# Optimization experiments

Measured on AMD Instinct MI355X. Metric: run time of the kernel, lower is better.

The kernel has to match this reference:

```python
import jax, jax.numpy as jnp
import numpy as np

B, N, IN_F, OUT_F = 32, 1024, 256, 256


def setup_inputs() -> dict:
    key = jax.random.key(0)
    k_adj, k_feat, k_w, k_b = jax.random.split(key, 4)
    adjacency = jax.random.uniform(k_adj, (B, N, N), dtype=jnp.float32)  # [B,N,N]
    features = jax.random.normal(k_feat, (B, N, IN_F), dtype=jnp.float32)  # [B,N,in]
    # 'thomas' init ~ uniform(-1/sqrt(fan_in), 1/sqrt(fan_in)) style; scale is
    # irrelevant to correctness-checking, use scaled normal.
    weight = jax.random.normal(k_w, (IN_F, OUT_F), dtype=jnp.float32) / np.sqrt(IN_F)
    bias = jax.random.normal(k_b, (OUT_F,), dtype=jnp.float32) / np.sqrt(IN_F)
    return {"adjacency": adjacency, "features": features, "weight": weight, "bias": bias}


def reference(adjacency, features, weight, bias) -> jnp.ndarray:
    # support = features @ weight : [B,N,out]
    support = jnp.einsum("bni,io->bno", features, weight)
    # output = bmm(adjacency, support) : [B,N,out]
    output = jnp.einsum("bnm,bmo->bno", adjacency, support)
    return output + bias
```

## Files before the change

kernel.cpp:

```cpp
#include <hip/hip_runtime.h>
#include <hip/hip_bf16.h>


typedef __attribute__((__ext_vector_type__(4))) float  f32x4;
typedef __attribute__((__ext_vector_type__(8))) __bf16 bf16x8;
typedef __attribute__((__ext_vector_type__(4))) __bf16 bf16x4;

#define BM 64
#define BN 256
#define BK 32

__device__ __forceinline__ void gld16(const void* g, void* l) {
  __builtin_amdgcn_global_load_lds(
      (const __attribute__((address_space(1))) unsigned int*)g,
      (__attribute__((address_space(3))) unsigned int*)l, 16, 0, 0);
}

__global__ __launch_bounds__(256) void k_wt(const float* __restrict__ w,
                                            __bf16* __restrict__ Wt) {
  __shared__ __bf16 T[64][65];
  const int bi = blockIdx.x >> 2;
  const int bj = blockIdx.x & 3;
  const int t  = threadIdx.x;
  const int r  = t >> 2;
  const int q  = t & 3;
  const float* src = w + (size_t)(bi * 64 + r) * 256 + bj * 64 + q * 16;
#pragma unroll
  for (int u = 0; u < 4; ++u) {
    f32x4 v = *(const f32x4*)(src + u * 4);
    T[r][q * 16 + u * 4 + 0] = (__bf16)v[0];
    T[r][q * 16 + u * 4 + 1] = (__bf16)v[1];
    T[r][q * 16 + u * 4 + 2] = (__bf16)v[2];
    T[r][q * 16 + u * 4 + 3] = (__bf16)v[3];
  }
  __syncthreads();
  bf16x8 h0, h1;
#pragma unroll
  for (int u = 0; u < 8; ++u) {
    h0[u] = T[q * 16 + u][r];
    h1[u] = T[q * 16 + 8 + u][r];
  }
  __bf16* d0 = Wt + ((size_t)(bi * 8 + q * 2) * 256 + (bj * 64 + r)) * 8;
  *(bf16x8*)d0          = h0;
  *(bf16x8*)(d0 + 2048) = h1;
}

template <int KTOT, int LDA, bool EPI_ST>
__global__ __launch_bounds__(512, 4) void k_gemm(
    const float* __restrict__ Aall, const __bf16* __restrict__ Bg_all,
    const float* __restrict__ bias, float* __restrict__ Out,
    __bf16* __restrict__ St) {
  __shared__ float  Af[2][BM * BK];
  __shared__ __bf16 Bf[2][4 * BN * 8];

  const int tid  = threadIdx.x;
  const int lane = tid & 63;
  const int wid  = tid >> 6;
  const int wr   = wid >> 2;
  const int wc   = wid & 3;
  const int l16  = lane & 15;
  const int g    = lane >> 4;

  int b, mtile;
  const float*  Ablk;
  const __bf16* Bblk;
  if constexpr (EPI_ST) {
    const int lg = blockIdx.x;
    b     = lg >> 4;
    mtile = lg & 15;
    Ablk  = Aall + (size_t)lg * BM * LDA;
    Bblk  = Bg_all;
  } else {
    const int h  = blockIdx.x;
    const int lg = (h & 7) * 64 + (h >> 3);
    b     = lg >> 4;
    mtile = lg & 15;
    Ablk  = Aall + (size_t)b * 1024 * 1024 + (size_t)mtile * BM * LDA;
    Bblk  = Bg_all + (size_t)b * 262144;
  }

  const int    ar   = tid >> 3;
  const float* asrc = Ablk + (size_t)ar * LDA + (((tid & 7) ^ (ar & 7)) << 2);
  const __bf16* bs0 = Bblk + ((size_t)wid * 128 + lane) * 8;

  auto stage = [&](int buf, int k0) {
    gld16(asrc + k0, &Af[buf][wid * 256]);
    const __bf16* bt = bs0 + (size_t)(k0 >> 3) * 2048;
    gld16(bt,       &Bf[buf][wid * 1024]);
    gld16(bt + 512, &Bf[buf][wid * 1024 + 512]);
  };

  f32x4 acc[2][4];
#pragma unroll
  for (int m = 0; m < 2; ++m)
#pragma unroll
    for (int n = 0; n < 4; ++n) acc[m][n] = (f32x4){0.f, 0.f, 0.f, 0.f};

  const int h7 = l16 & 7;
  auto compute = [&](int buf) {
    bf16x8 af[2], bv[4];
#pragma unroll
    for (int m = 0; m < 2; ++m) {
      const float* base = &Af[buf][(wr * 32 + m * 16 + l16) * BK];
      f32x4 v0 = *(const f32x4*)(base + (((2 * g)     ^ h7) << 2));
      f32x4 v1 = *(const f32x4*)(base + (((2 * g + 1) ^ h7) << 2));
      af[m] = (bf16x8){(__bf16)v0[0], (__bf16)v0[1], (__bf16)v0[2], (__bf16)v0[3],
                       (__bf16)v1[0], (__bf16)v1[1], (__bf16)v1[2], (__bf16)v1[3]};
    }
#pragma unroll
    for (int n = 0; n < 4; ++n)
      bv[n] = *(const bf16x8*)&Bf[buf][(g * 256 + wc * 64 + n * 16 + l16) * 8];
#pragma unroll
    for (int m = 0; m < 2; ++m)
#pragma unroll
      for (int n = 0; n < 4; ++n)
        acc[m][n] = __builtin_amdgcn_mfma_f32_16x16x32_bf16(af[m], bv[n], acc[m][n], 0, 0, 0);
  };

  constexpr int NT = KTOT / BK;
  stage(0, 0);
  __syncthreads();
  for (int t = 0; t < NT - 2; t += 2) {
    stage(1, (t + 1) * BK);
    compute(0);
    __syncthreads();
    stage(0, (t + 2) * BK);
    compute(1);
    __syncthreads();
  }
  stage(1, (NT - 1) * BK);
  compute(0);
  __syncthreads();
  compute(1);

  const int rg = (lane >> 4) * 4;
  if constexpr (EPI_ST) {
    __bf16* Stb = St + (size_t)b * 262144;
#pragma unroll
    for (int n = 0; n < 4; ++n) {
      const int col = wc * 64 + n * 16 + l16;
#pragma unroll
      for (int m = 0; m < 2; ++m) {
        const int gm = mtile * 64 + wr * 32 + m * 16 + rg;
        __bf16* dst = Stb + ((size_t)(gm >> 3) * 256 + col) * 8 + (gm & 7);
        bf16x4 hh = {(__bf16)acc[m][n][0], (__bf16)acc[m][n][1],
                     (__bf16)acc[m][n][2], (__bf16)acc[m][n][3]};
        *(bf16x4*)dst = hh;
      }
    }
  } else {
    float* ob = Out + ((size_t)b * 1024 + (size_t)mtile * BM) * 256;
#pragma unroll
    for (int n = 0; n < 4; ++n) {
      const int col = wc * 64 + n * 16 + l16;
      const float bvs = bias[col];
#pragma unroll
      for (int m = 0; m < 2; ++m) {
        const int row = wr * 32 + m * 16 + rg;
#pragma unroll
        for (int r2 = 0; r2 < 4; ++r2)
          ob[(size_t)(row + r2) * 256 + col] = acc[m][n][r2] + bvs;
      }
    }
  }
}

extern "C" void kernel_launch(void* const* d_in, const int* in_sizes, int n_in,
                              void* d_out, int out_size, void* d_ws, size_t ws_size,
                              hipStream_t stream) {
  const float* adj  = (const float*)d_in[0];
  const float* feat = (const float*)d_in[1];
  const float* w    = (const float*)d_in[2];
  const float* bias = (const float*)d_in[3];
  float* out = (float*)d_out;

  __bf16* Wt = (__bf16*)d_ws;
  __bf16* St = (__bf16*)((char*)d_ws + 131072);

  k_wt<<<16, 256, 0, stream>>>(w, Wt);
  k_gemm<256, 256, true><<<512, 512, 0, stream>>>(feat, Wt, nullptr, nullptr, St);
  k_gemm<1024, 1024, false><<<512, 512, 0, stream>>>(adj, St, bias, out, nullptr);
}
```

Measured before the change: 54.37 us.

## Replace LDS-staged GEMM with direct global-to-register double-buffered loads

New measurement: 73.33 us. 1.35x slower.

```diff
diff --git a/kernel.cpp b/kernel.cpp
--- a/kernel.cpp
+++ b/kernel.cpp
@@ -6,15 +6,7 @@
 typedef __attribute__((__ext_vector_type__(8))) __bf16 bf16x8;
 typedef __attribute__((__ext_vector_type__(4))) __bf16 bf16x4;
 
-#define BM 64
-#define BN 256
 #define BK 32
-
-__device__ __forceinline__ void gld16(const void* g, void* l) {
-  __builtin_amdgcn_global_load_lds(
-      (const __attribute__((address_space(1))) unsigned int*)g,
-      (__attribute__((address_space(3))) unsigned int*)l, 16, 0, 0);
-}
 
 __global__ __launch_bounds__(256) void k_wt(const float* __restrict__ w,
                                             __bf16* __restrict__ Wt) {
@@ -46,117 +38,113 @@
 }
 
 template <int KTOT, int LDA, bool EPI_ST>
-__global__ __launch_bounds__(512, 4) void k_gemm(
+__global__ __launch_bounds__(256, 2) void k_gemm(
     const float* __restrict__ Aall, const __bf16* __restrict__ Bg_all,
     const float* __restrict__ bias, float* __restrict__ Out,
     __bf16* __restrict__ St) {
-  __shared__ float  Af[2][BM * BK];
-  __shared__ __bf16 Bf[2][4 * BN * 8];
-
   const int tid  = threadIdx.x;
   const int lane = tid & 63;
-  const int wid  = tid >> 6;
-  const int wr   = wid >> 2;
-  const int wc   = wid & 3;
+  const int w    = tid >> 6;
   const int l16  = lane & 15;
   const int g    = lane >> 4;
 
-  int b, mtile;
+  int b, mblk;
   const float*  Ablk;
   const __bf16* Bblk;
   if constexpr (EPI_ST) {
-    const int lg = blockIdx.x;
-    b     = lg >> 4;
-    mtile = lg & 15;
-    Ablk  = Aall + (size_t)lg * BM * LDA;
-    Bblk  = Bg_all;
+    const int bx = blockIdx.x;
+    b    = bx >> 4;
+    mblk = bx & 15;
+    Ablk = Aall + (size_t)bx * 64 * LDA;
+    Bblk = Bg_all;
   } else {
     const int h  = blockIdx.x;
     const int lg = (h & 7) * 64 + (h >> 3);
-    b     = lg >> 4;
-    mtile = lg & 15;
-    Ablk  = Aall + (size_t)b * 1024 * 1024 + (size_t)mtile * BM * LDA;
-    Bblk  = Bg_all + (size_t)b * 262144;
+    b    = lg >> 4;
+    mblk = lg & 15;
+    Ablk = Aall + (size_t)b * 1024 * 1024 + (size_t)mblk * 64 * LDA;
+    Bblk = Bg_all + (size_t)b * 262144;
   }
 
-  const int    ar   = tid >> 3;
-  const float* asrc = Ablk + (size_t)ar * LDA + (((tid & 7) ^ (ar & 7)) << 2);
-  const __bf16* bs0 = Bblk + ((size_t)wid * 128 + lane) * 8;
+  const int wm = (w >> 1) * 32;
+  const int nb = (w & 1) * 128;
 
-  auto stage = [&](int buf, int k0) {
-    gld16(asrc + k0, &Af[buf][wid * 256]);
-    const __bf16* bt = bs0 + (size_t)(k0 >> 3) * 2048;
-    gld16(bt,       &Bf[buf][wid * 1024]);
-    gld16(bt + 512, &Bf[buf][wid * 1024 + 512]);
+  const float* arow0 = Ablk + (size_t)(wm + l16) * LDA + g * 8;
+  const float* arow1 = arow0 + (size_t)16 * LDA;
+  const __bf16* bl = Bblk + (size_t)g * 2048 + (size_t)(nb + l16) * 8;
+
+  f32x4  a0[4], a1[4];
+  bf16x8 b0[8], b1[8];
+
+  auto issueA = [&](f32x4* a, int k0) {
+    a[0] = *(const f32x4*)(arow0 + k0);
+    a[1] = *(const f32x4*)(arow0 + k0 + 4);
+    a[2] = *(const f32x4*)(arow1 + k0);
+    a[3] = *(const f32x4*)(arow1 + k0 + 4);
+  };
+  auto issueB = [&](bf16x8* bb, int k0) {
+    const __bf16* p = bl + (size_t)(k0 >> 3) * 2048;
+#pragma unroll
+    for (int n = 0; n < 8; ++n) bb[n] = *(const bf16x8*)(p + n * 128);
   };
 
-  f32x4 acc[2][4];
+  f32x4 acc[2][8];
 #pragma unroll
   for (int m = 0; m < 2; ++m)
 #pragma unroll
-    for (int n = 0; n < 4; ++n) acc[m][n] = (f32x4){0.f, 0.f, 0.f, 0.f};
+    for (int n = 0; n < 8; ++n) acc[m][n] = (f32x4){0.f, 0.f, 0.f, 0.f};
 
-  const int h7 = l16 & 7;
-  auto compute = [&](int buf) {
-    bf16x8 af[2], bv[4];
+  auto step = [&](const f32x4* a, const bf16x8* bb) {
+    bf16x8 af0 = {(__bf16)a[0][0], (__bf16)a[0][1], (__bf16)a[0][2], (__bf16)a[0][3],
+                  (__bf16)a[1][0], (__bf16)a[1][1], (__bf16)a[1][2], (__bf16)a[1][3]};
+    bf16x8 af1 = {(__bf16)a[2][0], (__bf16)a[2][1], (__bf16)a[2][2], (__bf16)a[2][3],
+                  (__bf16)a[3][0], (__bf16)a[3][1], (__bf16)a[3][2], (__bf16)a[3][3]};
 #pragma unroll
-    for (int m = 0; m < 2; ++m) {
-      const float* base = &Af[buf][(wr * 32 + m * 16 + l16) * BK];
-      f32x4 v0 = *(const f32x4*)(base + (((2 * g)     ^ h7) << 2));
-      f32x4 v1 = *(const f32x4*)(base + (((2 * g + 1) ^ h7) << 2));
-      af[m] = (bf16x8){(__bf16)v0[0], (__bf16)v0[1], (__bf16)v0[2], (__bf16)v0[3],
-                       (__bf16)v1[0], (__bf16)v1[1], (__bf16)v1[2], (__bf16)v1[3]};
+    for (int n = 0; n < 8; ++n) {
+      acc[0][n] = __builtin_amdgcn_mfma_f32_16x16x32_bf16(af0, bb[n], acc[0][n], 0, 0, 0);
+      acc[1][n] = __builtin_amdgcn_mfma_f32_16x16x32_bf16(af1, bb[n], acc[1][n], 0, 0, 0);
     }
-#pragma unroll
-    for (int n = 0; n < 4; ++n)
-      bv[n] = *(const bf16x8*)&Bf[buf][(g * 256 + wc * 64 + n * 16 + l16) * 8];
-#pragma unroll
-    for (int m = 0; m < 2; ++m)
-#pragma unroll
-      for (int n = 0; n < 4; ++n)
-        acc[m][n] = __builtin_amdgcn_mfma_f32_16x16x32_bf16(af[m], bv[n], acc[m][n], 0, 0, 0);
   };
 
   constexpr int NT = KTOT / BK;
-  stage(0, 0);
-  __syncthreads();
+  issueA(a0, 0);   issueB(b0, 0);
+  issueA(a1, BK);  issueB(b1, BK);
   for (int t = 0; t < NT - 2; t += 2) {
-    stage(1, (t + 1) * BK);
-    compute(0);
-    __syncthreads();
-    stage(0, (t + 2) * BK);
-    compute(1);
-    __syncthreads();
+    step(a0, b0);
+    issueA(a0, (t + 2) * BK);
+    issueB(b0, (t + 2) * BK);
+    step(a1, b1);
+    issueA(a1, (t + 3) * BK);
+    issueB(b1, (t + 3) * BK);
   }
-  stage(1, (NT - 1) * BK);
-  compute(0);
-  __syncthreads();
-  compute(1);
+  step(a0, b0);
+  step(a1, b1);
 
-  const int rg = (lane >> 4) * 4;
+  const int rg = g * 4;
   if constexpr (EPI_ST) {
     __bf16* Stb = St + (size_t)b * 262144;
+    const int gm0 = mblk * 64 + wm;
 #pragma unroll
-    for (int n = 0; n < 4; ++n) {
-      const int col = wc * 64 + n * 16 + l16;
+    for (int n = 0; n < 8; ++n) {
+      const int col = nb + n * 16 + l16;
 #pragma unroll
       for (int m = 0; m < 2; ++m) {
-        const int gm = mtile * 64 + wr * 32 + m * 16 + rg;
-        __bf16* dst = Stb + ((size_t)(gm >> 3) * 256 + col) * 8 + (gm & 7);
+        const int gm = gm0 + m * 16 + rg;
+        __bf16* dst = Stb + (size_t)(gm >> 3) * 2048 + (size_t)col * 8 + (gm & 7);
         bf16x4 hh = {(__bf16)acc[m][n][0], (__bf16)acc[m][n][1],
                      (__bf16)acc[m][n][2], (__bf16)acc[m][n][3]};
         *(bf16x4*)dst = hh;
       }
     }
   } else {
-    float* ob = Out + ((size_t)b * 1024 + (size_t)mtile * BM) * 256;
+    float* ob = Out + ((size_t)b * 1024 + (size_t)mblk * 64 + wm) * 256;
 #pragma unroll
-    for (int n = 0; n < 4; ++n) {
-      const int col = wc * 64 + n * 16 + l16;
+    for (int n = 0; n < 8; ++n) {
+      const int col = nb + n * 16 + l16;
       const float bvs = bias[col];
 #pragma unroll
       for (int m = 0; m < 2; ++m) {
-        const int row = wr * 32 + m * 16 + rg;
+        const int row = m * 16 + rg;
 #pragma unroll
         for (int r2 = 0; r2 < 4; ++r2)
           ob[(size_t)(row + r2) * 256 + col] = acc[m][n][r2] + bvs;
@@ -178,6 +166,6 @@
   __bf16* St = (__bf16*)((char*)d_ws + 131072);
 
   k_wt<<<16, 256, 0, stream>>>(w, Wt);
-  k_gemm<256, 256, true><<<512, 512, 0, stream>>>(feat, Wt, nullptr, nullptr, St);
-  k_gemm<1024, 1024, false><<<512, 512, 0, stream>>>(adj, St, bias, out, nullptr);
+  k_gemm<256, 256, true><<<512, 256, 0, stream>>>(feat, Wt, nullptr, nullptr, St);
+  k_gemm<1024, 1024, false><<<512, 256, 0, stream>>>(adj, St, bias, out, nullptr);
 }
```

## Enlarge GEMM tiles to 128x256 with BK=64 and halve grid size

Applied to the files above, without the earlier changes.

Measured after the change: 54.09 us. Within noise of the previous version (-0.5%).

```diff
diff --git a/kernel.cpp b/kernel.cpp
--- a/kernel.cpp
+++ b/kernel.cpp
@@ -6,9 +6,7 @@
 typedef __attribute__((__ext_vector_type__(8))) __bf16 bf16x8;
 typedef __attribute__((__ext_vector_type__(4))) __bf16 bf16x4;
 
-#define BM 64
-#define BN 256
-#define BK 32
+#define BK 64
 
 __device__ __forceinline__ void gld16(const void* g, void* l) {
   __builtin_amdgcn_global_load_lds(
@@ -46,12 +44,12 @@
 }
 
 template <int KTOT, int LDA, bool EPI_ST>
-__global__ __launch_bounds__(512, 4) void k_gemm(
+__global__ __launch_bounds__(512, 2) void k_gemm(
     const float* __restrict__ Aall, const __bf16* __restrict__ Bg_all,
     const float* __restrict__ bias, float* __restrict__ Out,
     __bf16* __restrict__ St) {
-  __shared__ float  Af[2][BM * BK];
-  __shared__ __bf16 Bf[2][4 * BN * 8];
+  __shared__ float  Af[2][128 * 64];
+  __shared__ __bf16 Bf[2][8 * 256 * 8];
 
   const int tid  = threadIdx.x;
   const int lane = tid & 63;
@@ -61,102 +59,118 @@
   const int l16  = lane & 15;
   const int g    = lane >> 4;
 
-  int b, mtile;
+  int b, mblk;
   const float*  Ablk;
   const __bf16* Bblk;
   if constexpr (EPI_ST) {
-    const int lg = blockIdx.x;
-    b     = lg >> 4;
-    mtile = lg & 15;
-    Ablk  = Aall + (size_t)lg * BM * LDA;
-    Bblk  = Bg_all;
+    const int bx = blockIdx.x;
+    b    = bx >> 3;
+    mblk = bx & 7;
+    Ablk = Aall + (size_t)bx * 128 * LDA;
+    Bblk = Bg_all;
   } else {
     const int h  = blockIdx.x;
-    const int lg = (h & 7) * 64 + (h >> 3);
-    b     = lg >> 4;
-    mtile = lg & 15;
-    Ablk  = Aall + (size_t)b * 1024 * 1024 + (size_t)mtile * BM * LDA;
-    Bblk  = Bg_all + (size_t)b * 262144;
+    const int lg = (h & 7) * 32 + (h >> 3);
+    b    = lg >> 3;
+    mblk = lg & 7;
+    Ablk = Aall + (size_t)b * 1024 * 1024 + (size_t)mblk * 128 * LDA;
+    Bblk = Bg_all + (size_t)b * 262144;
   }
 
-  const int    ar   = tid >> 3;
-  const float* asrc = Ablk + (size_t)ar * LDA + (((tid & 7) ^ (ar & 7)) << 2);
-  const __bf16* bs0 = Bblk + ((size_t)wid * 128 + lane) * 8;
+  const float*  aS[4];
+  const __bf16* bS[4];
+#pragma unroll
+  for (int i = 0; i < 4; ++i) {
+    const int c = i * 512 + tid;
+    aS[i] = Ablk + (size_t)(c >> 4) * LDA + (((c & 15) ^ ((c >> 4) & 7)) << 2);
+    bS[i] = Bblk + (size_t)c * 8;
+  }
 
-  auto stage = [&](int buf, int k0) {
-    gld16(asrc + k0, &Af[buf][wid * 256]);
-    const __bf16* bt = bs0 + (size_t)(k0 >> 3) * 2048;
-    gld16(bt,       &Bf[buf][wid * 1024]);
-    gld16(bt + 512, &Bf[buf][wid * 1024 + 512]);
-  };
+#define STAGE(buf, k0)                                                        \
+  {                                                                           \
+    const size_t koff = (size_t)((k0) >> 3) * 2048;                           \
+    _Pragma("unroll") for (int i = 0; i < 4; ++i) {                           \
+      gld16(aS[i] + (k0), &Af[buf][(i * 512 + wid * 64) * 4]);                \
+      gld16(bS[i] + koff, &Bf[buf][(i * 512 + wid * 64) * 8]);                \
+    }                                                                         \
+  }
 
-  f32x4 acc[2][4];
+  f32x4 acc[4][4];
 #pragma unroll
-  for (int m = 0; m < 2; ++m)
+  for (int m = 0; m < 4; ++m)
 #pragma unroll
     for (int n = 0; n < 4; ++n) acc[m][n] = (f32x4){0.f, 0.f, 0.f, 0.f};
 
-  const int h7 = l16 & 7;
   auto compute = [&](int buf) {
-    bf16x8 af[2], bv[4];
 #pragma unroll
-    for (int m = 0; m < 2; ++m) {
-      const float* base = &Af[buf][(wr * 32 + m * 16 + l16) * BK];
-      f32x4 v0 = *(const f32x4*)(base + (((2 * g)     ^ h7) << 2));
-      f32x4 v1 = *(const f32x4*)(base + (((2 * g + 1) ^ h7) << 2));
-      af[m] = (bf16x8){(__bf16)v0[0], (__bf16)v0[1], (__bf16)v0[2], (__bf16)v0[3],
-                       (__bf16)v1[0], (__bf16)v1[1], (__bf16)v1[2], (__bf16)v1[3]};
+    for (int ks = 0; ks < 2; ++ks) {
+      bf16x8 af[4], bv[4];
+#pragma unroll
+      for (int m = 0; m < 4; ++m) {
+        const int row = wr * 64 + m * 16 + l16;
+        const int rx  = row & 7;
+        const int c0  = (ks * 8 + 2 * g) ^ rx;
+        const int c1  = (ks * 8 + 2 * g + 1) ^ rx;
+        f32x4 v0 = *(const f32x4*)&Af[buf][row * 64 + c0 * 4];
+        f32x4 v1 = *(const f32x4*)&Af[buf][row * 64 + c1 * 4];
+        af[m] = (bf16x8){(__bf16)v0[0], (__bf16)v0[1], (__bf16)v0[2], (__bf16)v0[3],
+                         (__bf16)v1[0], (__bf16)v1[1], (__bf16)v1[2], (__bf16)v1[3]};
+      }
+#pragma unroll
+      for (int n = 0; n < 4; ++n) {
+        const int col = wc * 64 + n * 16 + l16;
+        bv[n] = *(const bf16x8*)&Bf[buf][((ks * 4 + g) * 256 + col) * 8];
+      }
+#pragma unroll
+      for (int m = 0; m < 4; ++m)
+#pragma unroll
+        for (int n = 0; n < 4; ++n)
+          acc[m][n] = __builtin_amdgcn_mfma_f32_16x16x32_bf16(af[m], bv[n], acc[m][n], 0, 0, 0);
     }
-#pragma unroll
-    for (int n = 0; n < 4; ++n)
-      bv[n] = *(const bf16x8*)&Bf[buf][(g * 256 + wc * 64 + n * 16 + l16) * 8];
-#pragma unroll
-    for (int m = 0; m < 2; ++m)
-#pragma unroll
-      for (int n = 0; n < 4; ++n)
-        acc[m][n] = __builtin_amdgcn_mfma_f32_16x16x32_bf16(af[m], bv[n], acc[m][n], 0, 0, 0);
   };
 
   constexpr int NT = KTOT / BK;
-  stage(0, 0);
+  STAGE(0, 0);
   __syncthreads();
   for (int t = 0; t < NT - 2; t += 2) {
-    stage(1, (t + 1) * BK);
+    STAGE(1, (t + 1) * BK);
     compute(0);
     __syncthreads();
-    stage(0, (t + 2) * BK);
+    STAGE(0, (t + 2) * BK);
     compute(1);
     __syncthreads();
   }
-  stage(1, (NT - 1) * BK);
+  STAGE(1, (NT - 1) * BK);
   compute(0);
   __syncthreads();
   compute(1);
+#undef STAGE
 
-  const int rg = (lane >> 4) * 4;
+  const int rg = g * 4;
   if constexpr (EPI_ST) {
     __bf16* Stb = St + (size_t)b * 262144;
+    const int gm0 = mblk * 128 + wr * 64;
 #pragma unroll
     for (int n = 0; n < 4; ++n) {
       const int col = wc * 64 + n * 16 + l16;
 #pragma unroll
-      for (int m = 0; m < 2; ++m) {
-        const int gm = mtile * 64 + wr * 32 + m * 16 + rg;
-        __bf16* dst = Stb + ((size_t)(gm >> 3) * 256 + col) * 8 + (gm & 7);
+      for (int m = 0; m < 4; ++m) {
+        const int gm = gm0 + m * 16 + rg;
+        __bf16* dst = Stb + (size_t)(gm >> 3) * 2048 + (size_t)col * 8 + (gm & 7);
         bf16x4 hh = {(__bf16)acc[m][n][0], (__bf16)acc[m][n][1],
                      (__bf16)acc[m][n][2], (__bf16)acc[m][n][3]};
         *(bf16x4*)dst = hh;
       }
     }
   } else {
-    float* ob = Out + ((size_t)b * 1024 + (size_t)mtile * BM) * 256;
+    float* ob = Out + ((size_t)b * 1024 + (size_t)mblk * 128 + wr * 64) * 256;
 #pragma unroll
     for (int n = 0; n < 4; ++n) {
       const int col = wc * 64 + n * 16 + l16;
       const float bvs = bias[col];
 #pragma unroll
-      for (int m = 0; m < 2; ++m) {
-        const int row = wr * 32 + m * 16 + rg;
+      for (int m = 0; m < 4; ++m) {
+        const int row = m * 16 + rg;
 #pragma unroll
         for (int r2 = 0; r2 < 4; ++r2)
           ob[(size_t)(row + r2) * 256 + col] = acc[m][n][r2] + bvs;
@@ -178,6 +192,6 @@
   __bf16* St = (__bf16*)((char*)d_ws + 131072);
 
   k_wt<<<16, 256, 0, stream>>>(w, Wt);
-  k_gemm<256, 256, true><<<512, 512, 0, stream>>>(feat, Wt, nullptr, nullptr, St);
-  k_gemm<1024, 1024, false><<<512, 512, 0, stream>>>(adj, St, bias, out, nullptr);
+  k_gemm<256, 256, true><<<256, 512, 0, stream>>>(feat, Wt, nullptr, nullptr, St);
+  k_gemm<1024, 1024, false><<<256, 512, 0, stream>>>(adj, St, bias, out, nullptr);
 }
```
